# Kernel tuning notes

Measured on AMD Instinct MI355X. Metric: run time of the kernel, lower is better.

The kernel has to match this reference:

```python
import jax, jax.numpy as jnp
import numpy as np

RADIUS = 50.0
EPS = 1e-8


def setup_inputs() -> dict:
    key = jax.random.key(0)
    k1, k2, k3, k4, k5 = jax.random.split(key, 5)
    N, E, H = 16384, 524288, 256
    x = jax.random.normal(k1, (N, H), dtype=jnp.float32)
    edge_index = jax.random.randint(k2, (2, E), 0, N, dtype=jnp.int32)
    spatial_coords = jax.random.uniform(k3, (N, 2), dtype=jnp.float32) * 1000.0
    w1 = jax.random.normal(k4, (3, H // 2), dtype=jnp.float32) * 0.02
    b1 = jnp.zeros((H // 2,), dtype=jnp.float32)
    w2 = jax.random.normal(k5, (H // 2, H), dtype=jnp.float32) * 0.02
    b2 = jnp.zeros((H,), dtype=jnp.float32)
    return {"x": x, "edge_index": edge_index, "spatial_coords": spatial_coords,
            "w1": w1, "b1": b1, "w2": w2, "b2": b2}


def reference(x, edge_index, spatial_coords, w1, b1, w2, b2):
    N = x.shape[0]
    row, col = edge_index[0], edge_index[1]

    # degree via scatter-add (segment_sum)
    ones = jnp.ones(row.shape, dtype=x.dtype)
    degree = jax.ops.segment_sum(ones, row, num_segments=N)  # [N]

    # spatial density: count neighbors within RADIUS (full pairwise, vectorized)
    sq = jnp.sum(spatial_coords * spatial_coords, axis=-1)  # [N]
    d2 = sq[:, None] + sq[None, :] - 2.0 * (spatial_coords @ spatial_coords.T)  # [N,N] squared dists
    in_radius = (d2 <= RADIUS * RADIUS).astype(x.dtype)
    density = jnp.sum(in_radius, axis=1) - 1.0  # exclude self
    density = density / (jnp.max(density) + EPS)

    # local feature variance: || x - mean(neighbor features) ||
    nbr_sum = jax.ops.segment_sum(x[col], row, num_segments=N)  # [N,H]
    cnt = jnp.clip(degree, 1.0)[:, None]
    nbr_mean = nbr_sum / cnt
    fvar = jnp.linalg.norm(x - nbr_mean, axis=-1)  # [N]
    fvar = fvar / (jnp.max(fvar) + EPS)

    feats = jnp.stack([degree / (jnp.max(degree) + EPS), density, fvar], axis=-1)  # [N,3]
    h = jax.nn.relu(feats @ w1 + b1)
    return h @ w2 + b2  # [N, hidden_dim]
```

## Files before the change

### kernel.cpp

```cpp
#include <hip/hip_runtime.h>
#include <math.h>

#define R2 2500.0f
#define EPSF 1e-8f

constexpr int H   = 256;
constexpr int HH  = 128;
constexpr int NB  = 8;
constexpr int BSH = 11;
constexpr int RPW = 4;

__global__ void __launch_bounds__(256) k_degcell(
    const int* __restrict__ row, const int* __restrict__ col,
    int* __restrict__ deg4, const float* __restrict__ coords,
    int* __restrict__ cellcnt, int E, int EB, int N) {
    if ((int)blockIdx.x < EB) {
        int e = blockIdx.x * 256 + threadIdx.x;
        if (e < E) atomicAdd(&deg4[row[e] * NB + (col[e] >> BSH)], 1);
    } else {
        int t = ((int)blockIdx.x - EB) * 256 + threadIdx.x;
        if (t < N) {
            float2 c = ((const float2*)coords)[t];
            int cx = (int)(c.x * 0.02f); if (cx > 19) cx = 19;
            int cy = (int)(c.y * 0.02f); if (cy > 19) cy = 19;
            atomicAdd(&cellcnt[cy * 20 + cx], 1);
        }
    }
}

__global__ void __launch_bounds__(256) k_bsum(const int* __restrict__ deg4,
                                              int* __restrict__ bsum) {
    int t = threadIdx.x;
    int4 v = ((const int4*)deg4)[blockIdx.x * 256 + t];
    int sum = v.x + v.y + v.z + v.w;
#pragma unroll
    for (int off = 32; off > 0; off >>= 1) sum += __shfl_xor(sum, off, 64);
    __shared__ int sw[4];
    if ((t & 63) == 0) sw[t >> 6] = sum;
    __syncthreads();
    if (t == 0) bsum[blockIdx.x] = sw[0] + sw[1] + sw[2] + sw[3];
}

__global__ void __launch_bounds__(512) k_scatcell(
    const int* __restrict__ deg4, const int* __restrict__ bsum,
    int* __restrict__ rp4, int* __restrict__ cur4, int M,
    const int* __restrict__ cellcnt, int* __restrict__ cellstart,
    int* __restrict__ cellcur) {
    __shared__ int s[512];
    int t = threadIdx.x;
    int blk = blockIdx.x;
    if (blk < gridDim.x - 1) {
        s[t] = (t < 128) ? bsum[t] : 0;
        __syncthreads();
        for (int off = 1; off < 128; off <<= 1) {
            int v = (t < 128) ? s[t] : 0;
            int add = (t >= off && t < 128) ? s[t - off] : 0;
            __syncthreads();
            if (t < 128) s[t] = v + add;
            __syncthreads();
        }
        int boff = (blk > 0) ? s[blk - 1] : 0;
        if (t < 256) {
            int lane = t & 63, w = t >> 6;
            int4 v = ((const int4*)deg4)[blk * 256 + t];
            int tsum = v.x + v.y + v.z + v.w;
            int incl = tsum;
#pragma unroll
            for (int off = 1; off < 64; off <<= 1) {
                int n = __shfl_up(incl, off, 64);
                if (lane >= off) incl += n;
            }
            __shared__ int wsum[4];
            if (lane == 63) wsum[w] = incl;
            __syncthreads();
            int woff = 0;
#pragma unroll
            for (int k = 0; k < 4; k++) woff += (k < w) ? wsum[k] : 0;
            int excl = boff + woff + (incl - tsum);
            int4 r;
            r.x = excl;
            r.y = excl + v.x;
            r.z = excl + v.x + v.y;
            r.w = excl + v.x + v.y + v.z;
            ((int4*)rp4)[blk * 256 + t]  = r;
            ((int4*)cur4)[blk * 256 + t] = r;
            if (blk == 127 && t == 255) rp4[M] = excl + tsum;
        }
    } else {
        s[t] = (t < 400) ? cellcnt[t] : 0;
        __syncthreads();
        for (int off = 1; off < 512; off <<= 1) {
            int v = s[t];
            int add = (t >= off) ? s[t - off] : 0;
            __syncthreads();
            s[t] = v + add;
            __syncthreads();
        }
        if (t < 400) {
            int excl = (t > 0) ? s[t - 1] : 0;
            cellstart[t] = excl;
            cellcur[t]   = excl;
        }
        if (t == 400) cellstart[400] = s[399];
    }
}

__global__ void __launch_bounds__(256) k_fillcell(
    const int* __restrict__ row, const int* __restrict__ col,
    int* __restrict__ cur4, int* __restrict__ cols,
    const float* __restrict__ coords, int* __restrict__ cellcur,
    float4* __restrict__ pts, int E, int EB, int N) {
    if ((int)blockIdx.x < EB) {
        int e = blockIdx.x * 256 + threadIdx.x;
        if (e < E) {
            int r = row[e], c = col[e];
            int p = atomicAdd(&cur4[r * NB + (c >> BSH)], 1);
            cols[p] = c;
        }
    } else {
        int t = ((int)blockIdx.x - EB) * 256 + threadIdx.x;
        if (t < N) {
            float2 c = ((const float2*)coords)[t];
            int cx = (int)(c.x * 0.02f); if (cx > 19) cx = 19;
            int cy = (int)(c.y * 0.02f); if (cy > 19) cy = 19;
            int p = atomicAdd(&cellcur[cy * 20 + cx], 1);
            pts[p] = make_float4(c.x, c.y, c.x * c.x + c.y * c.y, __int_as_float(t));
        }
    }
}

__global__ void __launch_bounds__(256) k_dgrid(
    const float4* __restrict__ pts, const int* __restrict__ cellstart,
    int* __restrict__ dens, int N) {
    int wave = threadIdx.x >> 6;
    int lane = threadIdx.x & 63;
    int t = blockIdx.x * 4 + wave;
    float4 p = pts[t];
    int cx = (int)(p.x * 0.02f); if (cx > 19) cx = 19;
    int cy = (int)(p.y * 0.02f); if (cy > 19) cy = 19;
    int x0 = cx - 2; if (x0 < 0) x0 = 0;
    int x1 = cx + 2; if (x1 > 19) x1 = 19;
    int y0 = cy - 2; if (y0 < 0) y0 = 0;
    int y1 = cy + 2; if (y1 > 19) y1 = 19;
    int cnt = 0;
    for (int yy = y0; yy <= y1; yy++) {
        int rowb = yy * 20;
        int s = cellstart[rowb + x0];
        int e = cellstart[rowb + x1 + 1];
        for (int q = s + lane; q < e; q += 64) {
            float4 pq = pts[q];
            float dot = p.x * pq.x + p.y * pq.y;
            float d2 = (p.z + pq.z) - 2.0f * dot;
            cnt += (d2 <= R2) ? 1 : 0;
        }
    }
#pragma unroll
    for (int off = 32; off > 0; off >>= 1) cnt += __shfl_xor(cnt, off, 64);
    if (lane == 0) dens[__float_as_int(p.w)] = cnt;
}

__global__ void __launch_bounds__(256, 4) k_fvar(
    const float* __restrict__ x, const int* __restrict__ rp4,
    const int* __restrict__ cols, float* __restrict__ fvar, int N) {
    int wave = threadIdx.x >> 6;
    int lane = threadIdx.x & 63;
    int i0 = (blockIdx.x * 4 + wave) * RPW;
    const float4* xb = (const float4*)x;

    int bnd = rp4[i0 * NB + (lane < 32 ? lane : 32)];

    float4 acc0 = make_float4(0.f, 0.f, 0.f, 0.f);
    float4 acc1 = make_float4(0.f, 0.f, 0.f, 0.f);
    float4 acc2 = make_float4(0.f, 0.f, 0.f, 0.f);
    float4 acc3 = make_float4(0.f, 0.f, 0.f, 0.f);

    for (int b = 0; b < NB; b++) {
#pragma unroll
        for (int r = 0; r < RPW; r++) {
            float4& a = (r == 0) ? acc0 : (r == 1) ? acc1 : (r == 2) ? acc2 : acc3;
            int s = __shfl(bnd, r * NB + b, 64);
            int e = __shfl(bnd, r * NB + b + 1, 64);
            for (int p0 = s; p0 < e; p0 += 64) {
                int m = e - p0; if (m > 64) m = 64;
                int idx = cols[p0 + (lane < m ? lane : m - 1)];
                for (int j = 0; j < m; j += 8) {
                    int nb2 = m - j; if (nb2 > 8) nb2 = 8;
                    float4 g0 = xb[(size_t)__shfl(idx, j + 0, 64) * 64 + lane];
                    float4 g1 = xb[(size_t)__shfl(idx, j + 1, 64) * 64 + lane];
                    float4 g2 = xb[(size_t)__shfl(idx, j + 2, 64) * 64 + lane];
                    float4 g3 = xb[(size_t)__shfl(idx, j + 3, 64) * 64 + lane];
                    float4 g4 = xb[(size_t)__shfl(idx, j + 4, 64) * 64 + lane];
                    float4 g5 = xb[(size_t)__shfl(idx, j + 5, 64) * 64 + lane];
                    float4 g6 = xb[(size_t)__shfl(idx, j + 6, 64) * 64 + lane];
                    float4 g7 = xb[(size_t)__shfl(idx, j + 7, 64) * 64 + lane];
                    float w0 = (1 < nb2 + 1) ? 1.0f : 0.0f;
                    float w1 = (1 < nb2) ? 1.0f : 0.0f;
                    float w2 = (2 < nb2) ? 1.0f : 0.0f;
                    float w3 = (3 < nb2) ? 1.0f : 0.0f;
                    float w4 = (4 < nb2) ? 1.0f : 0.0f;
                    float w5 = (5 < nb2) ? 1.0f : 0.0f;
                    float w6 = (6 < nb2) ? 1.0f : 0.0f;
                    float w7 = (7 < nb2) ? 1.0f : 0.0f;
                    a.x = fmaf(g0.x, w0, a.x); a.y = fmaf(g0.y, w0, a.y);
                    a.z = fmaf(g0.z, w0, a.z); a.w = fmaf(g0.w, w0, a.w);
                    a.x = fmaf(g1.x, w1, a.x); a.y = fmaf(g1.y, w1, a.y);
                    a.z = fmaf(g1.z, w1, a.z); a.w = fmaf(g1.w, w1, a.w);
                    a.x = fmaf(g2.x, w2, a.x); a.y = fmaf(g2.y, w2, a.y);
                    a.z = fmaf(g2.z, w2, a.z); a.w = fmaf(g2.w, w2, a.w);
                    a.x = fmaf(g3.x, w3, a.x); a.y = fmaf(g3.y, w3, a.y);
                    a.z = fmaf(g3.z, w3, a.z); a.w = fmaf(g3.w, w3, a.w);
                    a.x = fmaf(g4.x, w4, a.x); a.y = fmaf(g4.y, w4, a.y);
                    a.z = fmaf(g4.z, w4, a.z); a.w = fmaf(g4.w, w4, a.w);
                    a.x = fmaf(g5.x, w5, a.x); a.y = fmaf(g5.y, w5, a.y);
                    a.z = fmaf(g5.z, w5, a.z); a.w = fmaf(g5.w, w5, a.w);
                    a.x = fmaf(g6.x, w6, a.x); a.y = fmaf(g6.y, w6, a.y);
                    a.z = fmaf(g6.z, w6, a.z); a.w = fmaf(g6.w, w6, a.w);
                    a.x = fmaf(g7.x, w7, a.x); a.y = fmaf(g7.y, w7, a.y);
                    a.z = fmaf(g7.z, w7, a.z); a.w = fmaf(g7.w, w7, a.w);
                }
            }
        }
    }

#define FIN(RR, ACCR)                                                   \
    {                                                                   \
        int i = i0 + (RR);                                              \
        float cnt = fmaxf((float)(__shfl(bnd, (RR) * NB + NB, 64) -     \
                                  __shfl(bnd, (RR) * NB, 64)), 1.0f);   \
        float4 xi = xb[(size_t)i * 64 + lane];                          \
        float dx = xi.x - ACCR.x / cnt;                                 \
        float dy = xi.y - ACCR.y / cnt;                                 \
        float dz = xi.z - ACCR.z / cnt;                                 \
        float dw = xi.w - ACCR.w / cnt;                                 \
        float ss = dx * dx + dy * dy + dz * dz + dw * dw;               \
        _Pragma("unroll")                                               \
        for (int off = 32; off > 0; off >>= 1) ss += __shfl_xor(ss, off, 64); \
        if (lane == 0) fvar[i] = sqrtf(ss);                             \
    }

    FIN(0, acc0);
    FIN(1, acc1);
    FIN(2, acc2);
    FIN(3, acc3);
#undef FIN
}

__global__ void __launch_bounds__(256) k_scal(
    const int* __restrict__ rp4, const int* __restrict__ dens,
    const float* __restrict__ fvar, int* __restrict__ scal, int N) {
    __shared__ int sd[4], sn[4];
    __shared__ float sf[4];
    int t = threadIdx.x;
    int g = blockIdx.x * 256 + t;
    int stride = 256 * gridDim.x;
    int md = 0, mn = 0;
    float mf = 0.f;
    for (int i = g; i < N; i += stride) {
        md = max(md, rp4[(i + 1) * NB] - rp4[i * NB]);
        mn = max(mn, dens[i]);
        mf = fmaxf(mf, fvar[i]);
    }
#pragma unroll
    for (int off = 32; off > 0; off >>= 1) {
        md = max(md, __shfl_xor(md, off, 64));
        mn = max(mn, __shfl_xor(mn, off, 64));
        mf = fmaxf(mf, __shfl_xor(mf, off, 64));
    }
    int w = t >> 6, l = t & 63;
    if (l == 0) { sd[w] = md; sn[w] = mn; sf[w] = mf; }
    __syncthreads();
    if (t == 0) {
#pragma unroll
        for (int k = 1; k < 4; k++) {
            md = max(md, sd[k]);
            mn = max(mn, sn[k]);
            mf = fmaxf(mf, sf[k]);
        }
        atomicMax(&scal[0], md);
        atomicMax(&scal[1], mn);
        atomicMax(&scal[2], __float_as_int(mf));
    }
}

__global__ void __launch_bounds__(256) k_mlp(
    const float* __restrict__ w1, const float* __restrict__ b1,
    const float* __restrict__ w2, const float* __restrict__ b2,
    const int* __restrict__ rp4, const int* __restrict__ dens,
    const float* __restrict__ fvar, const int* __restrict__ scal,
    float* __restrict__ out, int N) {
    __shared__ float sh_h[HH];
    int j = threadIdx.x;
    float wv[HH];
#pragma unroll
    for (int l = 0; l < HH; l++) wv[l] = w2[l * H + j];
    float bj = b2[j];
    float maxdeg  = (float)scal[0] + EPSF;
    float maxdens = (float)(scal[1] - 1) + EPSF;
    float maxfv   = __int_as_float(scal[2]) + EPSF;
    float w1a = 0.f, w1b = 0.f, w1c = 0.f, b1j = 0.f;
    if (j < HH) { w1a = w1[j]; w1b = w1[HH + j]; w1c = w1[2 * HH + j]; b1j = b1[j]; }
    for (int i = blockIdx.x; i < N; i += gridDim.x) {
        float f0 = (float)(rp4[(i + 1) * NB] - rp4[i * NB]) / maxdeg;
        float f1 = (float)(dens[i] - 1) / maxdens;
        float f2 = fvar[i] / maxfv;
        if (j < HH) {
            float h = f0 * w1a + f1 * w1b + f2 * w1c + b1j;
            sh_h[j] = fmaxf(h, 0.0f);
        }
        __syncthreads();
        float acc = bj;
#pragma unroll
        for (int l = 0; l < HH; l++) acc = fmaf(sh_h[l], wv[l], acc);
        out[(size_t)i * H + j] = acc;
        __syncthreads();
    }
}

extern "C" void kernel_launch(void* const* d_in, const int* in_sizes, int n_in,
                              void* d_out, int out_size, void* d_ws, size_t ws_size,
                              hipStream_t stream) {
    const float* x      = (const float*)d_in[0];
    const int*   ei     = (const int*)d_in[1];
    const float* coords = (const float*)d_in[2];
    const float* w1     = (const float*)d_in[3];
    const float* b1     = (const float*)d_in[4];
    const float* w2     = (const float*)d_in[5];
    const float* b2     = (const float*)d_in[6];
    float* out = (float*)d_out;

    const int N = in_sizes[2] / 2;
    const int E = in_sizes[1] / 2;
    const int M = N * NB;
    const int NBLK = M / 1024;
    const int EB = (E + 255) / 256;
    const int CB = N / 256;
    const int* row = ei;
    const int* col = ei + E;

    int* ws        = (int*)d_ws;
    int* scal      = ws;
    int* deg4      = ws + 4;
    int* cellcnt   = ws + 4 + M;
    int* rp4       = ws + 408 + M;
    int* cur4      = rp4 + M + 4;
    int* cellstart = cur4 + M;
    int* cellcur   = cellstart + 404;
    int* dens_cnt  = cellcur + 400;
    float* fvarp   = (float*)(dens_cnt + N);
    int* bsum      = dens_cnt + 2 * N;
    int* boff      = bsum + 128;
    int* cols      = boff + 128;
    float4* pts    = (float4*)(cols + E);

    hipMemsetAsync(ws, 0, (size_t)(408 + M) * sizeof(int), stream);

    k_degcell<<<EB + CB, 256, 0, stream>>>(row, col, deg4, coords, cellcnt, E, EB, N);
    k_bsum<<<NBLK, 256, 0, stream>>>(deg4, bsum);
    k_scatcell<<<NBLK + 1, 512, 0, stream>>>(deg4, bsum, rp4, cur4, M,
                                             cellcnt, cellstart, cellcur);
    k_fillcell<<<EB + CB, 256, 0, stream>>>(row, col, cur4, cols,
                                            coords, cellcur, pts, E, EB, N);

    k_dgrid<<<N / 4, 256, 0, stream>>>(pts, cellstart, dens_cnt, N);

    k_fvar<<<N / (4 * RPW), 256, 0, stream>>>(x, rp4, cols, fvarp, N);

    k_scal<<<64, 256, 0, stream>>>(rp4, dens_cnt, fvarp, scal, N);

    k_mlp<<<1024, 256, 0, stream>>>(w1, b1, w2, b2, rp4, dens_cnt, fvarp, scal,
                                    out, N);
}
```

Measured before the change: 246.6 us.

## Halve rows per wave in fvar gather and raise occupancy, skip empty buckets

```diff
diff --git a/kernel.cpp b/kernel.cpp
--- a/kernel.cpp
+++ b/kernel.cpp
@@ -8,7 +8,7 @@
 constexpr int HH  = 128;
 constexpr int NB  = 8;
 constexpr int BSH = 11;
-constexpr int RPW = 4;
+constexpr int RPW = 2;
 
 __global__ void __launch_bounds__(256) k_degcell(
     const int* __restrict__ row, const int* __restrict__ col,
@@ -159,7 +159,7 @@
     if (lane == 0) dens[__float_as_int(p.w)] = cnt;
 }
 
-__global__ void __launch_bounds__(256, 4) k_fvar(
+__global__ void __launch_bounds__(256, 8) k_fvar(
     const float* __restrict__ x, const int* __restrict__ rp4,
     const int* __restrict__ cols, float* __restrict__ fvar, int N) {
     int wave = threadIdx.x >> 6;
@@ -167,33 +167,39 @@
     int i0 = (blockIdx.x * 4 + wave) * RPW;
     const float4* xb = (const float4*)x;
 
-    int bnd = rp4[i0 * NB + (lane < 32 ? lane : 32)];
+    int bnd = rp4[i0 * NB + (lane < 2 * NB ? lane : 2 * NB)];
 
     float4 acc0 = make_float4(0.f, 0.f, 0.f, 0.f);
     float4 acc1 = make_float4(0.f, 0.f, 0.f, 0.f);
-    float4 acc2 = make_float4(0.f, 0.f, 0.f, 0.f);
-    float4 acc3 = make_float4(0.f, 0.f, 0.f, 0.f);
 
     for (int b = 0; b < NB; b++) {
 #pragma unroll
         for (int r = 0; r < RPW; r++) {
-            float4& a = (r == 0) ? acc0 : (r == 1) ? acc1 : (r == 2) ? acc2 : acc3;
+            float4& a = (r == 0) ? acc0 : acc1;
             int s = __shfl(bnd, r * NB + b, 64);
             int e = __shfl(bnd, r * NB + b + 1, 64);
+            if (e <= s) continue;
             for (int p0 = s; p0 < e; p0 += 64) {
                 int m = e - p0; if (m > 64) m = 64;
                 int idx = cols[p0 + (lane < m ? lane : m - 1)];
                 for (int j = 0; j < m; j += 8) {
                     int nb2 = m - j; if (nb2 > 8) nb2 = 8;
-                    float4 g0 = xb[(size_t)__shfl(idx, j + 0, 64) * 64 + lane];
-                    float4 g1 = xb[(size_t)__shfl(idx, j + 1, 64) * 64 + lane];
-                    float4 g2 = xb[(size_t)__shfl(idx, j + 2, 64) * 64 + lane];
-                    float4 g3 = xb[(size_t)__shfl(idx, j + 3, 64) * 64 + lane];
-                    float4 g4 = xb[(size_t)__shfl(idx, j + 4, 64) * 64 + lane];
-                    float4 g5 = xb[(size_t)__shfl(idx, j + 5, 64) * 64 + lane];
-                    float4 g6 = xb[(size_t)__shfl(idx, j + 6, 64) * 64 + lane];
-                    float4 g7 = xb[(size_t)__shfl(idx, j + 7, 64) * 64 + lane];
-                    float w0 = (1 < nb2 + 1) ? 1.0f : 0.0f;
+                    size_t o0 = (size_t)__shfl(idx, j + 0, 64) * 64 + lane;
+                    size_t o1 = (1 < nb2) ? (size_t)__shfl(idx, j + 1, 64) * 64 + lane : 0;
+                    size_t o2 = (2 < nb2) ? (size_t)__shfl(idx, j + 2, 64) * 64 + lane : 0;
+                    size_t o3 = (3 < nb2) ? (size_t)__shfl(idx, j + 3, 64) * 64 + lane : 0;
+                    size_t o4 = (4 < nb2) ? (size_t)__shfl(idx, j + 4, 64) * 64 + lane : 0;
+                    size_t o5 = (5 < nb2) ? (size_t)__shfl(idx, j + 5, 64) * 64 + lane : 0;
+                    size_t o6 = (6 < nb2) ? (size_t)__shfl(idx, j + 6, 64) * 64 + lane : 0;
+                    size_t o7 = (7 < nb2) ? (size_t)__shfl(idx, j + 7, 64) * 64 + lane : 0;
+                    float4 g0 = xb[o0];
+                    float4 g1 = xb[o1];
+                    float4 g2 = xb[o2];
+                    float4 g3 = xb[o3];
+                    float4 g4 = xb[o4];
+                    float4 g5 = xb[o5];
+                    float4 g6 = xb[o6];
+                    float4 g7 = xb[o7];
                     float w1 = (1 < nb2) ? 1.0f : 0.0f;
                     float w2 = (2 < nb2) ? 1.0f : 0.0f;
                     float w3 = (3 < nb2) ? 1.0f : 0.0f;
@@ -201,8 +207,7 @@
                     float w5 = (5 < nb2) ? 1.0f : 0.0f;
                     float w6 = (6 < nb2) ? 1.0f : 0.0f;
                     float w7 = (7 < nb2) ? 1.0f : 0.0f;
-                    a.x = fmaf(g0.x, w0, a.x); a.y = fmaf(g0.y, w0, a.y);
-                    a.z = fmaf(g0.z, w0, a.z); a.w = fmaf(g0.w, w0, a.w);
+                    a.x += g0.x; a.y += g0.y; a.z += g0.z; a.w += g0.w;
                     a.x = fmaf(g1.x, w1, a.x); a.y = fmaf(g1.y, w1, a.y);
                     a.z = fmaf(g1.z, w1, a.z); a.w = fmaf(g1.w, w1, a.w);
                     a.x = fmaf(g2.x, w2, a.x); a.y = fmaf(g2.y, w2, a.y);
@@ -240,8 +245,6 @@
 
     FIN(0, acc0);
     FIN(1, acc1);
-    FIN(2, acc2);
-    FIN(3, acc3);
 #undef FIN
 }
 
```

Result: slower. 253.7 us (+2.9%).
